# Performance work log

Hardware: AMD Instinct MI355X
Metric: run time of the kernel (lower is better)

The kernel has to match this reference:

```python
import jax, jax.numpy as jnp
import numpy as np

# Dims matching init_kwargs / input_specs
H = 64   # latent_size (GRU hidden)
L = 64   # rnn_layers
D = 128  # input_size
B = 128  # batch
T = 256  # sequence length


def setup_inputs() -> dict:
    key = jax.random.key(0)
    ks = jax.random.split(key, 13)
    s = 1.0 / np.sqrt(H)  # PyTorch GRU/Linear default init scale
    u = lambda k, shp: jax.random.uniform(k, shp, jnp.float32, -s, s)
    return {
        "context": jax.random.normal(ks[0], (B, T, D), jnp.float32),
        # encoder GRU params; layer 0 consumes D, layers 1..L-1 consume H
        "enc_Wih0": u(ks[1], (3 * H, D)),
        "enc_Wih": u(ks[2], (L - 1, 3 * H, H)),
        "enc_Whh": u(ks[3], (L, 3 * H, H)),
        "enc_bih": u(ks[4], (L, 3 * H)),
        "enc_bhh": u(ks[5], (L, 3 * H)),
        # decoder GRU params
        "dec_Wih0": u(ks[6], (3 * H, D)),
        "dec_Wih": u(ks[7], (L - 1, 3 * H, H)),
        "dec_Whh": u(ks[8], (L, 3 * H, H)),
        "dec_bih": u(ks[9], (L, 3 * H)),
        "dec_bhh": u(ks[10], (L, 3 * H)),
        # output projection
        "Wo": u(ks[11], (D, H)),
        "bo": u(ks[12], (D,)),
    }


def _gru_cell(x, h, Wih, Whh, bih, bhh):
    # PyTorch gate order: r, z, n
    gi = x @ Wih.T + bih            # (B, 3H)
    gh = h @ Whh.T + bhh            # (B, 3H)
    ir, iz, inn = jnp.split(gi, 3, axis=-1)
    hr, hz, hn = jnp.split(gh, 3, axis=-1)
    r = jax.nn.sigmoid(ir + hr)
    z = jax.nn.sigmoid(iz + hz)
    n = jnp.tanh(inn + r * hn)
    return (1.0 - z) * n + z * h


def _run_gru(X, h0, Wih0, Wih, Whh, bih, bhh):
    # X: (B, T, D); h0: (L, B, H). Returns (top-layer outputs (B,T,H), final hidden (L,B,H)).
    def layer_step(x_in, lp):
        h_prev, W_ih, W_hh, b_i, b_h = lp
        h_new = _gru_cell(x_in, h_prev, W_ih, W_hh, b_i, b_h)
        return h_new, h_new

    @jax.checkpoint
    def step(hs, x_t):
        h_first = _gru_cell(x_t, hs[0], Wih0, Whh[0], bih[0], bhh[0])
        top, hs_rest = jax.lax.scan(
            layer_step, h_first, (hs[1:], Wih, Whh[1:], bih[1:], bhh[1:]))
        return jnp.concatenate([h_first[None], hs_rest], axis=0), top

    hs_final, outs = jax.lax.scan(step, h0, jnp.swapaxes(X, 0, 1))
    return jnp.swapaxes(outs, 0, 1), hs_final


def reference(context, enc_Wih0, enc_Wih, enc_Whh, enc_bih, enc_bhh,
              dec_Wih0, dec_Wih, dec_Whh, dec_bih, dec_bhh, Wo, bo):
    Bc = context.shape[0]
    h0 = jnp.zeros((L, Bc, H), context.dtype)
    # encoder: only final hidden state is used
    _, h_n = _run_gru(context, h0, enc_Wih0, enc_Wih, enc_Whh, enc_bih, enc_bhh)
    # teacher forcing (ratio=1.0): decoder input at step i is X[:, i-1], zeros at i=0
    dec_in = jnp.concatenate([jnp.zeros_like(context[:, :1]), context[:, :-1]], axis=1)
    dec_out, _ = _run_gru(dec_in, h_n, dec_Wih0, dec_Wih, dec_Whh, dec_bih, dec_bhh)
    return dec_out @ Wo.T + bo  # (B, T, D)
```

## Files before the change

### kernel.cpp

```cpp
#include <hip/hip_runtime.h>
#include <stdint.h>

typedef uint16_t u16;
typedef unsigned long long u64;
typedef __attribute__((ext_vector_type(8))) short short8;
typedef __attribute__((ext_vector_type(4))) float f32x4;

#define SCOPE __HIP_MEMORY_SCOPE_AGENT
#define FSTRIDE 16
#define FLD(p) __hip_atomic_load((p), __ATOMIC_RELAXED, SCOPE)
#define FST(p, v) __hip_atomic_store((p), (v), __ATOMIC_RELAXED, SCOPE)

template <int N> struct IC { static constexpr int value = N; };

static __device__ __forceinline__ float bf2f(u16 b) {
  union { uint32_t u; float f; } x; x.u = ((uint32_t)b) << 16; return x.f;
}
static __device__ __forceinline__ u16 f2bf(float f) {
  union { float f; uint32_t u; } x; x.f = f;
  uint32_t u = x.u;
  u += 0x7fffu + ((u >> 16) & 1u);
  return (u16)(u >> 16);
}
static __device__ __forceinline__ float sigm(float x) {
  return __builtin_amdgcn_rcpf(1.f + __expf(-x));
}
static __device__ __forceinline__ float tanhf_(float x) {
  return 1.f - 2.f * __builtin_amdgcn_rcpf(1.f + __expf(2.f * x));
}
static __device__ __forceinline__ void lds_barrier() {
  asm volatile("s_waitcnt lgkmcnt(0)\n\ts_barrier" ::: "memory");
}
#define DRAIN0() asm volatile("s_waitcnt vmcnt(0)" ::: "memory")
static __device__ __forceinline__ int imin(int a, int b) { return a < b ? a : b; }

#define OFF_WHA 0
#define OFF_WHB 12288
#define OFF_WIB 24576
#define OFF_WIA 36864
#define OFF_WO  49152

template <int CHE, int CHD>
__global__ __launch_bounds__(512, 1) void gru_pipeline(
    const void* ctx_,
    const void* eWih0_, const void* eWih_, const void* eWhh_,
    const void* ebih_,  const void* ebhh_,
    const void* dWih0_, const void* dWih_, const void* dWhh_,
    const void* dbih_,  const void* dbhh_,
    const void* Wo_,    const void* bo_,   void* out_,
    int* __restrict__ pflag, int* __restrict__ cflag,
    u64* __restrict__ xbufW, int RW, int RE)
{
  const int tid  = threadIdx.x;
  const bool isX = (tid < 256);
  const int lane = tid & 63;
  const int qg   = (tid >> 6) & 3;
  const int w8   = tid >> 6;
  const int lo   = lane & 15;
  const int hi   = lane >> 4;
  const int blk  = blockIdx.x;
  const int P    = blk >> 3;
  const int g    = blk & 7;
  const int LA   = 2 * P;
  const int NKCA = (P == 0) ? 4 : 2;
  u64* xbufE = (u64*)out_;

  extern __shared__ __align__(16) u16 dynlds[];

  __shared__ __align__(16) u16 hbA[2][16 * 72];
  __shared__ __align__(16) u16 hbB[2][16 * 72];
  __shared__ __align__(16) u16 xstA[2][16 * 72];
  __shared__ int s_cnt, s_fin, s_cn;
  if (tid == 0) { s_cnt = 0; s_fin = 0; s_cn = 0; }
  for (int i = tid; i < 16 * 72; i += 512) {
    hbA[0][i] = 0; hbA[1][i] = 0; hbB[0][i] = 0; hbB[1][i] = 0;
    xstA[0][i] = 0; xstA[1][i] = 0;
  }
  __syncthreads();
  {
    u16 v = ((const u16*)ebih_)[2 * (tid & 255)];
    int e = (v >> 7) & 0xFF;
    if (e >= 100 && e <= 126 && isX) atomicAdd(&s_cnt, 1);
  }
  __syncthreads();
  const bool bf = (s_cnt >= 128);

  auto ld8 = [&](const void* p, int idx) -> short8 {
    if (bf) return *(const short8*)((const u16*)p + idx);
    const float* f = (const float*)p + idx;
    short8 r;
#pragma unroll
    for (int j = 0; j < 8; ++j) r[j] = (short)f2bf(f[j]);
    return r;
  };
  auto ld1 = [&](const void* p, int idx) -> float {
    return bf ? bf2f(((const u16*)p)[idx]) : ((const float*)p)[idx];
  };

  const int T0 = qg, T1 = 4 + qg, T2 = 8 + qg;

  short8 zf8 = {0,0,0,0,0,0,0,0};
  float  bov[2] = {0.f, 0.f};
  float brzA[2] = {0,0}, binA = 0, bhnA = 0;
  float brzB[2] = {0,0}, binB = 0, bhnB = 0;

  auto stage_w = [&](int offU16, const void* W, int gidx0, int NT, int KC, int K) {
    for (int nt = w8; nt < NT; nt += 8)
      for (int kc = 0; kc < KC; ++kc) {
        short8 v = ld8(W, gidx0 + (nt*16 + lo)*K + kc*32 + hi*8);
        *(short8*)(dynlds + offU16 + (nt*KC + kc)*512 + lane*8) = v;
      }
  };

  auto load_phase = [&](int ph) {
    const void* WH  = ph ? dWhh_ : eWhh_;
    const void* WIs = ph ? dWih_ : eWih_;
    const void* WI0 = ph ? dWih0_ : eWih0_;
    const void* bi  = ph ? dbih_ : ebih_;
    const void* bh  = ph ? dbhh_ : ebhh_;
    stage_w(OFF_WHA, WH, LA*192*64, 12, 2, 64);
    stage_w(OFF_WHB, WH, (LA+1)*192*64, 12, 2, 64);
    stage_w(OFF_WIB, WIs, LA*192*64, 12, 2, 64);
    if (LA == 0) stage_w(OFF_WIA, WI0, 0, 12, 4, 128);
    else         stage_w(OFF_WIA, WIs, (LA-1)*192*64, 12, 2, 64);
    if (isX) {
      brzA[0] = ld1(bi, LA*192 + T0*16 + lo) + ld1(bh, LA*192 + T0*16 + lo);
      brzA[1] = ld1(bi, LA*192 + T1*16 + lo) + ld1(bh, LA*192 + T1*16 + lo);
      binA    = ld1(bi, LA*192 + T2*16 + lo);
      bhnA    = ld1(bh, LA*192 + T2*16 + lo);
    } else {
      const int LB = LA + 1;
      brzB[0] = ld1(bi, LB*192 + T0*16 + lo) + ld1(bh, LB*192 + T0*16 + lo);
      brzB[1] = ld1(bi, LB*192 + T1*16 + lo) + ld1(bh, LB*192 + T1*16 + lo);
      binB    = ld1(bi, LB*192 + T2*16 + lo);
      bhnB    = ld1(bh, LB*192 + T2*16 + lo);
    }
  };
  load_phase(0);
  if (P == 31) {
    stage_w(OFF_WO, Wo_, 0, 8, 2, 64);
    if (!isX) { bov[0] = ld1(bo_, 32*qg + lo); bov[1] = ld1(bo_, 32*qg + 16 + lo); }
  }

  const int oWhA0 = OFF_WHA + T0*1024 + lane*8;
  const int oWhA1 = OFF_WHA + T1*1024 + lane*8;
  const int oWhA2 = OFF_WHA + T2*1024 + lane*8;
  const int oWhB0 = OFF_WHB + T0*1024 + lane*8;
  const int oWhB1 = OFF_WHB + T1*1024 + lane*8;
  const int oWhB2 = OFF_WHB + T2*1024 + lane*8;
  const int oWiB0 = OFF_WIB + T0*1024 + lane*8;
  const int oWiB1 = OFF_WIB + T1*1024 + lane*8;
  const int oWiB2 = OFF_WIB + T2*1024 + lane*8;
  const int oWiA0 = OFF_WIA + T0*(NKCA*512) + lane*8;
  const int oWiA1 = OFF_WIA + T1*(NKCA*512) + lane*8;
  const int oWiA2 = OFF_WIA + T2*(NKCA*512) + lane*8;
  const int oWo0  = OFF_WO + (2*qg + 0)*1024 + lane*8;
  const int oWo1  = OFF_WO + (2*qg + 1)*1024 + lane*8;

  auto WF = [&](int off, int kc) -> short8 {
    return *(const short8*)(dynlds + off + kc*512);
  };

  auto do_proj = [&](int tprev, const u16* hs) {
    f32x4 pacc[2];
#pragma unroll
    for (int ct = 0; ct < 2; ++ct) { float v = bov[ct]; f32x4 tv = {v,v,v,v}; pacc[ct] = tv; }
#pragma unroll
    for (int kc = 0; kc < 2; ++kc) {
      short8 hA = *(const short8*)(hs + lo*72 + kc*32 + hi*8);
      pacc[0] = __builtin_amdgcn_mfma_f32_16x16x32_bf16(hA, WF(oWo0, kc), pacc[0], 0, 0, 0);
      pacc[1] = __builtin_amdgcn_mfma_f32_16x16x32_bf16(hA, WF(oWo1, kc), pacc[1], 0, 0, 0);
    }
#pragma unroll
    for (int ct = 0; ct < 2; ++ct) {
      int n = 32*qg + 16*ct + lo;
#pragma unroll
      for (int p = 0; p < 4; ++p) {
        int b = 16*g + hi*4 + p;
        size_t idx = ((size_t)b * 256 + (tprev - 256)) * 128 + n;
        float v = fminf(64.f, fmaxf(-64.f, pacc[ct][p]));
        if (bf) ((u16*)out_)[idx] = f2bf(v);
        else    ((float*)out_)[idx] = v;
      }
    }
  };

  float hprevA[4] = {0,0,0,0}, hprevB[4] = {0,0,0,0};
  const int brow = 16*g + lo;

  const int eIn  = (P > 0 ? P - 1 : 0) * 8 + g;
  const int eOut = (P < 31 ? P : 30) * 8 + g;
  int* fin   = pflag + eIn  * FSTRIDE;
  int* fout  = pflag + eOut * FSTRIDE;
  int* cself = cflag + (P * 8 + g) * FSTRIDE;
  int* cnext = cflag + ((P < 31 ? P + 1 : 31) * 8 + g) * FSTRIDE;

  auto raddr = [&](int t) -> const u64* {
    return (t < 256)
      ? (xbufE + (size_t)eIn * ((size_t)RE * 256) + (size_t)(t & (RE-1)) * 256)
      : (xbufW + (size_t)eIn * ((size_t)RW * 256) + (size_t)((t-256) & (RW-1)) * 256);
  };
  auto waddr = [&](int t) -> u64* {
    return (t < 256)
      ? (xbufE + (size_t)eOut * ((size_t)RE * 256) + (size_t)(t & (RE-1)) * 256)
      : (xbufW + (size_t)eOut * ((size_t)RW * 256) + (size_t)((t-256) & (RW-1)) * 256);
  };

  int budget = 1 << 22;
  const int srow = 4 * (tid & 3);
  const int scol = tid >> 2;

  int f0=0,f1=0,f2=0,f3=0, c0=0,c1=0,c2=0,c3=0;
  short8 cfx[4] = {zf8, zf8, zf8, zf8};

  auto doB = [&](int s) {
    f32x4 br, bz, bin2, bhn;
    { float v;
      v = brzB[0]; br   = (f32x4){v,v,v,v};
      v = brzB[1]; bz   = (f32x4){v,v,v,v};
      v = binB;    bin2 = (f32x4){v,v,v,v};
      v = bhnB;    bhn  = (f32x4){v,v,v,v}; }
    const u16* hsB = hbB[(s + 1) & 1];
    const u16* xsB = hbA[s & 1];
#pragma unroll
    for (int kc = 0; kc < 2; ++kc) {
      short8 hB = *(const short8*)(hsB + lo*72 + kc*32 + hi*8);
      short8 xB = *(const short8*)(xsB + lo*72 + kc*32 + hi*8);
      br   = __builtin_amdgcn_mfma_f32_16x16x32_bf16(hB, WF(oWhB0, kc), br,   0, 0, 0);
      bz   = __builtin_amdgcn_mfma_f32_16x16x32_bf16(hB, WF(oWhB1, kc), bz,   0, 0, 0);
      bhn  = __builtin_amdgcn_mfma_f32_16x16x32_bf16(hB, WF(oWhB2, kc), bhn,  0, 0, 0);
      br   = __builtin_amdgcn_mfma_f32_16x16x32_bf16(xB, WF(oWiB0, kc), br,   0, 0, 0);
      bz   = __builtin_amdgcn_mfma_f32_16x16x32_bf16(xB, WF(oWiB1, kc), bz,   0, 0, 0);
      bin2 = __builtin_amdgcn_mfma_f32_16x16x32_bf16(xB, WF(oWiB2, kc), bin2, 0, 0, 0);
    }
    u16 hBb[4];
#pragma unroll
    for (int p = 0; p < 4; ++p) {
      float r = sigm(br[p]);
      float z = sigm(bz[p]);
      float n = tanhf_(bin2[p] + r * bhn[p]);
      float h = n + z * (hprevB[p] - n);
      h = fminf(1.f, fmaxf(-1.f, h));
      hprevB[p] = h;
      hBb[p] = f2bf(h);
    }
    u16* hd = hbB[s & 1];
#pragma unroll
    for (int p = 0; p < 4; ++p)
      hd[(hi*4 + p) * 72 + qg*16 + lo] = hBb[p];
    if (P < 31) {
      u64 da = (u64)hBb[0] | ((u64)hBb[1] << 16) | ((u64)hBb[2] << 32) | ((u64)hBb[3] << 48);
      FST(waddr(s) + (16*qg + lo)*4 + hi, da);
    }
  };

  __syncthreads();

  auto span = [&](auto chc, const int tbase, const int cbase, const int RC, const bool dec) {
    constexpr int CH  = decltype(chc)::value;
    constexpr int PTT = (CH >= 2) ? CH - 2 : 0;
    const int NC = 256 / CH;

    if (P > 0) {
      if (tid == 0) {
        int v = s_fin;
        if (v < cbase + 1) {
          while (budget > 0) {
            int a = FLD(fin+0), b = FLD(fin+1), c = FLD(fin+2), d = FLD(fin+3);
            v = imin(imin(a, b), imin(c, d));
            if (v >= cbase + 1) break;
            --budget; __builtin_amdgcn_s_sleep(2);
          }
          s_fin = v;
        }
      }
      __syncthreads();
      if (isX) {
        u64 r0 = FLD(raddr(tbase) + tid);
        u16* xd = xstA[tbase & 1];
#pragma unroll
        for (int p = 0; p < 4; ++p) xd[(srow + p) * 72 + scol] = (u16)(r0 >> (16 * p));
      }
    }
    if (P == 0 && isX) {
      int tx = (tbase < 256) ? tbase : 0;
#pragma unroll
      for (int kc = 0; kc < 4; ++kc) cfx[kc] = ld8(ctx_, (brow*256 + tx)*128 + kc*32 + hi*8);
    }

#pragma unroll 1
    for (int k = 0; k < NC; ++k) {
      const int t0 = tbase + k * CH;
      const int ck = cbase + k;
      const int fneed = ck + 2 - ((dec && k == NC - 1) ? 1 : 0);
      const int need  = (k >= RC) ? (ck + 1 - RC) : 0;
      u64 ra[CH];
#pragma unroll
      for (int j = 0; j < CH; ++j) ra[j] = 0;

#pragma unroll
      for (int tt = 0; tt < CH; ++tt) {
        const int t = t0 + tt;
        lds_barrier();

        if (tt == 0) {
          int vf = s_fin, vc = s_cn;
          const bool slowF = (P > 0)  && (vf < fneed);
          const bool slowC = (P < 31) && (need > 0) && (vc < need);
          if (slowF || slowC) {
            if (tid == 0) {
              if (slowF) {
                int v = 0;
                while (budget > 0) {
                  int a = FLD(fin+0), b = FLD(fin+1), c = FLD(fin+2), d = FLD(fin+3);
                  v = imin(imin(a, b), imin(c, d));
                  if (v >= fneed) break;
                  --budget; __builtin_amdgcn_s_sleep(2);
                }
                s_fin = v;
              }
              if (slowC) {
                int v = 0;
                while (budget > 0) {
                  int a = FLD(cnext+0), b = FLD(cnext+1), c = FLD(cnext+2), d = FLD(cnext+3);
                  v = imin(imin(a, b), imin(c, d));
                  if (v >= need) break;
                  --budget; __builtin_amdgcn_s_sleep(2);
                }
                s_cn = v;
              }
            }
            lds_barrier();
          }
          if (isX && P > 0) {
#pragma unroll
            for (int j = 0; j < CH; ++j)
              if (t0 + 1 + j <= 511) ra[j] = FLD(raddr(t0 + 1 + j) + tid);
          }
        }

        if (isX) {
          if (tt == CH - 1 && tid == 0) {
            if (P > 0)  s_fin = imin(imin(f0, f1), imin(f2, f3));
            if (P < 31) s_cn  = imin(imin(c0, c1), imin(c2, c3));
          }
          if (tt == PTT && tid == 0) {
            if (P > 0)  { f0 = FLD(fin+0); f1 = FLD(fin+1); f2 = FLD(fin+2); f3 = FLD(fin+3); }
            if (P < 31) { c0 = FLD(cnext+0); c1 = FLD(cnext+1); c2 = FLD(cnext+2); c3 = FLD(cnext+3); }
          }

          f32x4 ar, az, ain, ahn;
          { float v;
            v = brzA[0]; ar  = (f32x4){v,v,v,v};
            v = brzA[1]; az  = (f32x4){v,v,v,v};
            v = binA;    ain = (f32x4){v,v,v,v};
            v = bhnA;    ahn = (f32x4){v,v,v,v}; }
          const u16* hsA = hbA[(t + 1) & 1];
#pragma unroll
          for (int kc = 0; kc < 2; ++kc) {
            short8 hA = *(const short8*)(hsA + lo*72 + kc*32 + hi*8);
            ar  = __builtin_amdgcn_mfma_f32_16x16x32_bf16(hA, WF(oWhA0, kc), ar,  0, 0, 0);
            az  = __builtin_amdgcn_mfma_f32_16x16x32_bf16(hA, WF(oWhA1, kc), az,  0, 0, 0);
            ahn = __builtin_amdgcn_mfma_f32_16x16x32_bf16(hA, WF(oWhA2, kc), ahn, 0, 0, 0);
          }
          short8 xfA[4] = {zf8, zf8, zf8, zf8};
          if (P > 0) {
            const u16* xs = xstA[t & 1];
#pragma unroll
            for (int kc = 0; kc < 2; ++kc)
              xfA[kc] = *(const short8*)(xs + lo*72 + kc*32 + hi*8);
          } else {
#pragma unroll
            for (int kc = 0; kc < 4; ++kc) xfA[kc] = cfx[kc];
          }
          if (!(P == 0 && t == 256)) {
#pragma unroll
            for (int kc = 0; kc < 4; ++kc) {
              if (kc < NKCA) {
                ar  = __builtin_amdgcn_mfma_f32_16x16x32_bf16(xfA[kc], WF(oWiA0, kc), ar,  0, 0, 0);
                az  = __builtin_amdgcn_mfma_f32_16x16x32_bf16(xfA[kc], WF(oWiA1, kc), az,  0, 0, 0);
                ain = __builtin_amdgcn_mfma_f32_16x16x32_bf16(xfA[kc], WF(oWiA2, kc), ain, 0, 0, 0);
              }
            }
          }
          u16 hAb[4];
#pragma unroll
          for (int p = 0; p < 4; ++p) {
            float r = sigm(ar[p]);
            float z = sigm(az[p]);
            float n = tanhf_(ain[p] + r * ahn[p]);
            float h = n + z * (hprevA[p] - n);
            h = fminf(1.f, fmaxf(-1.f, h));
            hprevA[p] = h;
            hAb[p] = f2bf(h);
          }
          {
            u16* hd = hbA[t & 1];
#pragma unroll
            for (int p = 0; p < 4; ++p)
              hd[(hi*4 + p) * 72 + qg*16 + lo] = hAb[p];
          }
          if (P == 0) {
            int tn = t + 1;
            if (tn <= 511) {
              int tx = (tn < 256) ? tn : ((tn == 256) ? 0 : tn - 257);
#pragma unroll
              for (int kc = 0; kc < 4; ++kc)
                cfx[kc] = ld8(ctx_, (brow*256 + tx)*128 + kc*32 + hi*8);
            }
          }
          if (P > 0 && t < 511) {
            u64 r = ra[tt];
            u16* xd = xstA[(t + 1) & 1];
#pragma unroll
            for (int p = 0; p < 4; ++p) xd[(srow + p) * 72 + scol] = (u16)(r >> (16 * p));
          }
          if (tt == CH - 1 && P > 0) {
            DRAIN0();
            if (lane == 0) FST(cself + qg, ck + 1);
          }
        } else {
          if (P == 31 && dec && t >= 258) do_proj(t - 2, hbB[t & 1]);
          if (t - 1 >= tbase) doB(t - 1);
          if (P < 31 && tt == 0 && k > 0) {
            DRAIN0();
            if (lane == 0) FST(fout + qg, ck);
          }
        }
      }
    }

    lds_barrier();
    if (!isX) {
      doB(tbase + 255);
      if (P < 31) {
        DRAIN0();
        if (lane == 0) FST(fout + qg, cbase + NC);
      }
    }
  };

  span(IC<CHE>{}, 0, 0, RE / CHE, false);
  __syncthreads();
  load_phase(1);
  __syncthreads();
  {
    int rcd = RW / CHD; if (rcd < 1) rcd = 1;
    span(IC<CHD>{}, 256, 256 / CHE, rcd, true);
  }

  lds_barrier();
  if (P == 31 && !isX) {
    do_proj(510, hbB[0]);
    do_proj(511, hbB[1]);
  }
}

extern "C" void kernel_launch(void* const* d_in, const int* in_sizes, int n_in,
                              void* d_out, int out_size, void* d_ws, size_t ws_size,
                              hipStream_t stream)
{
  char* ws = (char*)d_ws;
  int* pflag = (int*)ws;
  int* cflag = (int*)(ws + 16384);
  u64* xbufW = (u64*)(ws + 32768);

  const size_t per_slot = (size_t)31 * 8 * 2048;
  size_t avail = (ws_size > 32768) ? ws_size - 32768 : 0;
  int RW = 1;
  for (int r = 128; r >= 1; r >>= 1)
    if ((size_t)r * per_slot <= avail) { RW = r; break; }
  int RE = 1;
  for (int r = 16; r >= 1; r >>= 1)
    if ((size_t)r * per_slot <= (size_t)out_size) { RE = r; break; }

  const int dyn = 122880;
  static int attr_done = 0;
  if (!attr_done) {
    hipFuncSetAttribute(reinterpret_cast<const void*>(gru_pipeline<2,4>),
                        hipFuncAttributeMaxDynamicSharedMemorySize, dyn);
    hipFuncSetAttribute(reinterpret_cast<const void*>(gru_pipeline<2,2>),
                        hipFuncAttributeMaxDynamicSharedMemorySize, dyn);
    hipFuncSetAttribute(reinterpret_cast<const void*>(gru_pipeline<2,1>),
                        hipFuncAttributeMaxDynamicSharedMemorySize, dyn);
    attr_done = 1;
  }

  hipMemsetAsync(ws, 0, 32768, stream);

#define LAUNCH(CE, CD)                                                     \
  gru_pipeline<CE, CD><<<256, 512, dyn, stream>>>(                         \
      d_in[0], d_in[1], d_in[2], d_in[3], d_in[4], d_in[5],                \
      d_in[6], d_in[7], d_in[8], d_in[9], d_in[10], d_in[11], d_in[12],    \
      d_out, pflag, cflag, xbufW, RW, RE)

  if      (RW >= 16) LAUNCH(2, 4);
  else if (RW >= 8)  LAUNCH(2, 2);
  else               LAUNCH(2, 1);
#undef LAUNCH
  (void)in_sizes; (void)n_in;
}
```

Baseline: 1.708 ms.

## Move encoder ring to workspace, enlarge rings, relax credit flow control and chunking

Encoder inter-layer ring buffers move from the output tensor into a larger workspace region so both encoder and decoder rings can hold up to 256 slots. When the ring covers the whole sequence, consumer-to-producer credit signalling is disabled entirely. Flag polling now happens every step instead of once per chunk, and the producer-done flag is published earlier in the chunk. Chunk size can grow to 4 for both phases. This trades workspace memory and more frequent flag loads for fewer stalls on the cross-block pipeline.

```diff
diff --git a/kernel.cpp b/kernel.cpp
--- a/kernel.cpp
+++ b/kernel.cpp
@@ -49,7 +49,7 @@
     const void* dbih_,  const void* dbhh_,
     const void* Wo_,    const void* bo_,   void* out_,
     int* __restrict__ pflag, int* __restrict__ cflag,
-    u64* __restrict__ xbufW, int RW, int RE)
+    u64* __restrict__ ringE, u64* __restrict__ ringD, int RE, int RW)
 {
   const int tid  = threadIdx.x;
   const bool isX = (tid < 256);
@@ -63,7 +63,6 @@
   const int g    = blk & 7;
   const int LA   = 2 * P;
   const int NKCA = (P == 0) ? 4 : 2;
-  u64* xbufE = (u64*)out_;
 
   extern __shared__ __align__(16) u16 dynlds[];
 
@@ -197,13 +196,13 @@
 
   auto raddr = [&](int t) -> const u64* {
     return (t < 256)
-      ? (xbufE + (size_t)eIn * ((size_t)RE * 256) + (size_t)(t & (RE-1)) * 256)
-      : (xbufW + (size_t)eIn * ((size_t)RW * 256) + (size_t)((t-256) & (RW-1)) * 256);
+      ? (ringE + (size_t)eIn * ((size_t)RE * 256) + (size_t)(t & (RE-1)) * 256)
+      : (ringD + (size_t)eIn * ((size_t)RW * 256) + (size_t)((t-256) & (RW-1)) * 256);
   };
   auto waddr = [&](int t) -> u64* {
     return (t < 256)
-      ? (xbufE + (size_t)eOut * ((size_t)RE * 256) + (size_t)(t & (RE-1)) * 256)
-      : (xbufW + (size_t)eOut * ((size_t)RW * 256) + (size_t)((t-256) & (RW-1)) * 256);
+      ? (ringE + (size_t)eOut * ((size_t)RE * 256) + (size_t)(t & (RE-1)) * 256)
+      : (ringD + (size_t)eOut * ((size_t)RW * 256) + (size_t)((t-256) & (RW-1)) * 256);
   };
 
   int budget = 1 << 22;
@@ -257,9 +256,9 @@
   __syncthreads();
 
   auto span = [&](auto chc, const int tbase, const int cbase, const int RC, const bool dec) {
-    constexpr int CH  = decltype(chc)::value;
-    constexpr int PTT = (CH >= 2) ? CH - 2 : 0;
+    constexpr int CH = decltype(chc)::value;
     const int NC = 256 / CH;
+    const bool credOn = (RC < NC);
 
     if (P > 0) {
       if (tid == 0) {
@@ -271,7 +270,7 @@
             if (v >= cbase + 1) break;
             --budget; __builtin_amdgcn_s_sleep(2);
           }
-          s_fin = v;
+          s_fin = v; f0 = v; f1 = v; f2 = v; f3 = v;
         }
       }
       __syncthreads();
@@ -293,7 +292,7 @@
       const int t0 = tbase + k * CH;
       const int ck = cbase + k;
       const int fneed = ck + 2 - ((dec && k == NC - 1) ? 1 : 0);
-      const int need  = (k >= RC) ? (ck + 1 - RC) : 0;
+      const int need  = (credOn && k >= RC) ? (ck + 1 - RC) : 0;
       u64 ra[CH];
 #pragma unroll
       for (int j = 0; j < CH; ++j) ra[j] = 0;
@@ -317,7 +316,7 @@
                   if (v >= fneed) break;
                   --budget; __builtin_amdgcn_s_sleep(2);
                 }
-                s_fin = v;
+                s_fin = v; f0 = v; f1 = v; f2 = v; f3 = v;
               }
               if (slowC) {
                 int v = 0;
@@ -327,7 +326,7 @@
                   if (v >= need) break;
                   --budget; __builtin_amdgcn_s_sleep(2);
                 }
-                s_cn = v;
+                s_cn = v; c0 = v; c1 = v; c2 = v; c3 = v;
               }
             }
             lds_barrier();
@@ -340,13 +339,11 @@
         }
 
         if (isX) {
-          if (tt == CH - 1 && tid == 0) {
+          if (tid == 0) {
             if (P > 0)  s_fin = imin(imin(f0, f1), imin(f2, f3));
-            if (P < 31) s_cn  = imin(imin(c0, c1), imin(c2, c3));
-          }
-          if (tt == PTT && tid == 0) {
+            if (P < 31 && credOn) s_cn = imin(imin(c0, c1), imin(c2, c3));
             if (P > 0)  { f0 = FLD(fin+0); f1 = FLD(fin+1); f2 = FLD(fin+2); f3 = FLD(fin+3); }
-            if (P < 31) { c0 = FLD(cnext+0); c1 = FLD(cnext+1); c2 = FLD(cnext+2); c3 = FLD(cnext+3); }
+            if (P < 31 && credOn) { c0 = FLD(cnext+0); c1 = FLD(cnext+1); c2 = FLD(cnext+2); c3 = FLD(cnext+3); }
           }
 
           f32x4 ar, az, ain, ahn;
@@ -415,17 +412,18 @@
 #pragma unroll
             for (int p = 0; p < 4; ++p) xd[(srow + p) * 72 + scol] = (u16)(r >> (16 * p));
           }
-          if (tt == CH - 1 && P > 0) {
+          if (tt == CH - 1 && P > 0 && credOn) {
             DRAIN0();
             if (lane == 0) FST(cself + qg, ck + 1);
           }
         } else {
+          constexpr int FO = (CH >= 2) ? 1 : 0;
+          if (P < 31 && tt == FO && k > ((CH == 1) ? 1 : 0)) {
+            DRAIN0();
+            if (lane == 0) FST(fout + qg, ck - ((CH == 1) ? 1 : 0));
+          }
           if (P == 31 && dec && t >= 258) do_proj(t - 2, hbB[t & 1]);
           if (t - 1 >= tbase) doB(t - 1);
-          if (P < 31 && tt == 0 && k > 0) {
-            DRAIN0();
-            if (lane == 0) FST(fout + qg, ck);
-          }
         }
       }
     }
@@ -440,13 +438,15 @@
     }
   };
 
-  span(IC<CHE>{}, 0, 0, RE / CHE, false);
-  __syncthreads();
-  load_phase(1);
-  __syncthreads();
   {
-    int rcd = RW / CHD; if (rcd < 1) rcd = 1;
-    span(IC<CHD>{}, 256, 256 / CHE, rcd, true);
+    const int NCe = 256 / CHE;
+    int RCe = (RE >= 256) ? NCe : (RE / CHE) - 2; if (RCe < 1) RCe = 1;
+    span(IC<CHE>{}, 0, 0, RCe, false);
+    __syncthreads();
+    load_phase(1);
+    __syncthreads();
+    int RCd = (RW >= 256) ? (256 / CHD) : (RW / CHD) - 2; if (RCd < 1) RCd = 1;
+    span(IC<CHD>{}, 256, NCe, RCd, true);
   }
 
   lds_barrier();
@@ -462,41 +462,65 @@
 {
   char* ws = (char*)d_ws;
   int* pflag = (int*)ws;
-  int* cflag = (int*)(ws + 16384);
-  u64* xbufW = (u64*)(ws + 32768);
+  int* cflag = (int*)(ws + 32768);
+  char* ringbase = ws + 65536;
 
   const size_t per_slot = (size_t)31 * 8 * 2048;
-  size_t avail = (ws_size > 32768) ? ws_size - 32768 : 0;
-  int RW = 1;
-  for (int r = 128; r >= 1; r >>= 1)
-    if ((size_t)r * per_slot <= avail) { RW = r; break; }
-  int RE = 1;
-  for (int r = 16; r >= 1; r >>= 1)
-    if ((size_t)r * per_slot <= (size_t)out_size) { RE = r; break; }
+  size_t avail = (ws_size > 65536) ? ws_size - 65536 : 0;
+
+  int RE, RW;
+  u64 *ringE, *ringD;
+  int Rh = 0;
+  for (int r = 256; r >= 16; r >>= 1)
+    if ((size_t)(2 * r) * per_slot <= avail) { Rh = r; break; }
+  if (Rh) {
+    RE = RW = Rh;
+    ringE = (u64*)ringbase;
+    ringD = (u64*)(ringbase + (size_t)Rh * per_slot);
+  } else {
+    int Rw = 1;
+    for (int r = 256; r >= 1; r >>= 1)
+      if ((size_t)r * per_slot <= avail) { Rw = r; break; }
+    RW = Rw;
+    int Re = 1;
+    for (int r = 16; r >= 1; r >>= 1)
+      if ((size_t)r * per_slot <= (size_t)out_size) { Re = r; break; }
+    RE = Re;
+    ringE = (u64*)d_out;
+    ringD = (u64*)ringbase;
+  }
+  const int CHe = (RE >= 32) ? 4 : ((RE >= 16) ? 2 : 1);
+  const int CHd = (RW >= 32) ? 4 : ((RW >= 16) ? 2 : 1);
 
   const int dyn = 122880;
   static int attr_done = 0;
   if (!attr_done) {
+    hipFuncSetAttribute(reinterpret_cast<const void*>(gru_pipeline<4,4>),
+                        hipFuncAttributeMaxDynamicSharedMemorySize, dyn);
     hipFuncSetAttribute(reinterpret_cast<const void*>(gru_pipeline<2,4>),
                         hipFuncAttributeMaxDynamicSharedMemorySize, dyn);
     hipFuncSetAttribute(reinterpret_cast<const void*>(gru_pipeline<2,2>),
                         hipFuncAttributeMaxDynamicSharedMemorySize, dyn);
     hipFuncSetAttribute(reinterpret_cast<const void*>(gru_pipeline<2,1>),
                         hipFuncAttributeMaxDynamicSharedMemorySize, dyn);
+    hipFuncSetAttribute(reinterpret_cast<const void*>(gru_pipeline<1,1>),
+                        hipFuncAttributeMaxDynamicSharedMemorySize, dyn);
     attr_done = 1;
   }
 
-  hipMemsetAsync(ws, 0, 32768, stream);
+  hipMemsetAsync(ws, 0, 65536, stream);
 
 #define LAUNCH(CE, CD)                                                     \
   gru_pipeline<CE, CD><<<256, 512, dyn, stream>>>(                         \
       d_in[0], d_in[1], d_in[2], d_in[3], d_in[4], d_in[5],                \
       d_in[6], d_in[7], d_in[8], d_in[9], d_in[10], d_in[11], d_in[12],    \
-      d_out, pflag, cflag, xbufW, RW, RE)
-
-  if      (RW >= 16) LAUNCH(2, 4);
-  else if (RW >= 8)  LAUNCH(2, 2);
-  else               LAUNCH(2, 1);
+      d_out, pflag, cflag, ringE, ringD, RE, RW)
+
+  if      (CHe == 4 && CHd == 4) LAUNCH(4, 4);
+  else if (CHe == 2 && CHd == 4) LAUNCH(2, 4);
+  else if (CHe == 2 && CHd == 2) LAUNCH(2, 2);
+  else if (CHe == 2 && CHd == 1) LAUNCH(2, 1);
+  else                           LAUNCH(1, 1);
 #undef LAUNCH
   (void)in_sizes; (void)n_in;
 }
```

Result: slower. 1.861 ms (+8.9%).
